# Optimization experiments

Measured on AMD Instinct MI355X. Metric: run time of the kernel, lower is better.

The kernel has to match this reference:

```python
import jax, jax.numpy as jnp
import numpy as np

FRAME_LEN = 512
HOP_LEN = 128
FFT_SIZE = 512
N_SAMPLES = -1  # TF slice [:, :-1] drops the final sample
B, FRAMES, BINS = 16, 4000, FFT_SIZE // 2 + 1


def _inverse_window():
    # tf.signal.hann_window (periodic): 0.5 - 0.5*cos(2*pi*n/N)
    n = jnp.arange(FRAME_LEN, dtype=jnp.float32)
    win = 0.5 - 0.5 * jnp.cos(2.0 * np.pi * n / FRAME_LEN)
    # tf.signal.inverse_stft_window_fn: divide by overlap-added squared window
    denom = win * win
    overlaps = -(-FRAME_LEN // HOP_LEN)  # ceil div
    denom = jnp.pad(denom, (0, overlaps * HOP_LEN - FRAME_LEN))
    denom = denom.reshape(overlaps, HOP_LEN).sum(axis=0)  # [HOP_LEN]
    denom = jnp.tile(denom, overlaps)[:FRAME_LEN]
    return win / denom


def setup_inputs() -> dict:
    key = jax.random.key(0)
    k1, k2 = jax.random.split(key)
    return {
        "stft_real": jax.random.normal(k1, (B, FRAMES, BINS), dtype=jnp.float32),
        "stft_imag": jax.random.normal(k2, (B, FRAMES, BINS), dtype=jnp.float32),
    }


def reference(stft_real, stft_imag):
    stfts = jax.lax.complex(stft_real, stft_imag)  # [B, F, BINS] complex64
    # per-frame inverse real FFT, truncate to frame_length
    frames = jnp.fft.irfft(stfts, n=FFT_SIZE, axis=-1)[..., :FRAME_LEN]  # [B, F, L] float32
    frames = frames * _inverse_window()  # broadcast window over [B, F, L]
    out_len = (FRAMES - 1) * HOP_LEN + FRAME_LEN
    # overlap-add via vectorized scatter-accumulate
    idx = jnp.arange(FRAMES)[:, None] * HOP_LEN + jnp.arange(FRAME_LEN)[None, :]  # [F, L]
    sig = jnp.zeros((B, out_len), dtype=jnp.float32).at[:, idx].add(frames)
    return sig[:, :N_SAMPLES]
```

## Files before the change

kernel.cpp:

```cpp
#include <hip/hip_runtime.h>
#include <math.h>

#define HOP       128
#define NFFT      512
#define NBINS     257
#define NFRAMES   4000
#define NB        16
#define OUT_LEN   512383
#define CPR       16
#define RPB       251
#define NCHUNK    4003
#define SP        66
#define SQ        65
#define PBUF      528

__device__ __forceinline__ void dft8_inv(const float* xr, const float* xi,
                                         float* yr, float* yi)
{
    const float C = 0.70710678118654752f;
    float ar[8], ai[8];
    ar[0]=xr[0]+xr[4]; ai[0]=xi[0]+xi[4];
    ar[1]=xr[1]+xr[5]; ai[1]=xi[1]+xi[5];
    ar[2]=xr[2]+xr[6]; ai[2]=xi[2]+xi[6];
    ar[3]=xr[3]+xr[7]; ai[3]=xi[3]+xi[7];
    float t0r=xr[0]-xr[4], t0i=xi[0]-xi[4];
    float t1r=xr[1]-xr[5], t1i=xi[1]-xi[5];
    float t2r=xr[2]-xr[6], t2i=xi[2]-xi[6];
    float t3r=xr[3]-xr[7], t3i=xi[3]-xi[7];
    ar[4]= t0r;            ai[4]= t0i;
    ar[5]= C*(t1r-t1i);    ai[5]= C*(t1r+t1i);
    ar[6]=-t2i;            ai[6]= t2r;
    ar[7]=-C*(t3r+t3i);    ai[7]= C*(t3r-t3i);
    float br[8], bi[8];
    br[0]=ar[0]+ar[2]; bi[0]=ai[0]+ai[2];
    br[1]=ar[1]+ar[3]; bi[1]=ai[1]+ai[3];
    br[2]=ar[0]-ar[2]; bi[2]=ai[0]-ai[2];
    { float u=ar[1]-ar[3], v=ai[1]-ai[3]; br[3]=-v; bi[3]=u; }
    br[4]=ar[4]+ar[6]; bi[4]=ai[4]+ai[6];
    br[5]=ar[5]+ar[7]; bi[5]=ai[5]+ai[7];
    br[6]=ar[4]-ar[6]; bi[6]=ai[4]-ai[6];
    { float u=ar[5]-ar[7], v=ai[5]-ai[7]; br[7]=-v; bi[7]=u; }
    yr[0]=br[0]+br[1]; yi[0]=bi[0]+bi[1];
    yr[4]=br[0]-br[1]; yi[4]=bi[0]-bi[1];
    yr[2]=br[2]+br[3]; yi[2]=bi[2]+bi[3];
    yr[6]=br[2]-br[3]; yi[6]=bi[2]-bi[3];
    yr[1]=br[4]+br[5]; yi[1]=bi[4]+bi[5];
    yr[5]=br[4]-br[5]; yi[5]=bi[4]-bi[5];
    yr[3]=br[6]+br[7]; yi[3]=bi[6]+bi[7];
    yr[7]=br[6]-br[7]; yi[7]=bi[6]-bi[7];
}

__global__ __launch_bounds__(256)
void istft_r8_kernel(const float* __restrict__ re,
                     const float* __restrict__ im,
                     float* __restrict__ out)
{
    __shared__ float  wtab[NFFT];
    __shared__ float2 pbuf[4][PBUF];

    const int tid = threadIdx.x;
    const int wv  = tid >> 6;
    const int l   = tid & 63;

    for (int n = tid; n < NFFT; n += 256) {
        const float wn = 0.5f - 0.5f * __cosf(6.2831853071795864f * (float)n * (1.0f/512.0f));
        const int p = n & (HOP - 1);
        float denom = 0.0f;
        #pragma unroll
        for (int o = 0; o < 4; ++o) {
            const float w2 = 0.5f - 0.5f * __cosf(6.2831853071795864f * (float)(o*HOP + p) * (1.0f/512.0f));
            denom += w2 * w2;
        }
        wtab[n] = wn / (512.0f * denom);
    }
    __syncthreads();

    float2* P = pbuf[wv];

    const int rid = blockIdx.x * 4 + wv;
    const int b   = rid / RPB;
    const int rr  = rid - b * RPB;
    const int c0  = rr * CPR;
    const int fend = min(c0 + CPR - 1, NCHUNK - 1);

    const float* __restrict__ reb = re + (size_t)b * NFRAMES * NBINS;
    const float* __restrict__ imb = im + (size_t)b * NFRAMES * NBINS;
    float* __restrict__ outb = out + (size_t)b * OUT_LEN;

    float s1r[8], s1i[8];
    {
        float sr, cr;
        __sincosf(6.2831853071795864f * (float)l * (1.0f/512.0f), &sr, &cr);
        s1r[0] = 1.0f; s1i[0] = 0.0f; s1r[1] = cr; s1i[1] = sr;
        #pragma unroll
        for (int k = 2; k < 8; ++k) {
            s1r[k] = s1r[k-1]*cr - s1i[k-1]*sr;
            s1i[k] = s1r[k-1]*sr + s1i[k-1]*cr;
        }
    }
    float s2r[8], s2i[8];
    {
        float sr, cr;
        __sincosf(6.2831853071795864f * (float)(l & 7) * (1.0f/64.0f), &sr, &cr);
        s2r[0] = 1.0f; s2i[0] = 0.0f; s2r[1] = cr; s2i[1] = sr;
        #pragma unroll
        for (int k = 2; k < 8; ++k) {
            s2r[k] = s2r[k-1]*cr - s2i[k-1]*sr;
            s2i[k] = s2r[k-1]*sr + s2i[k-1]*cr;
        }
    }
    float ww[8];
    #pragma unroll
    for (int m1 = 0; m1 < 8; ++m1) ww[m1] = wtab[l + 64*m1];

    float acc[8];
    #pragma unroll
    for (int r = 0; r < 8; ++r) acc[r] = 0.0f;

    const int n0s = l >> 3, gs = l & 7;
    const int m0t = l >> 3, n0t = l & 7;

    for (int f = c0 - 3; f <= fend; ++f) {
        if (f >= 0 && f < NFRAMES) {
            const float* __restrict__ rb = reb + (size_t)f * NBINS;
            const float* __restrict__ ib = imb + (size_t)f * NBINS;

            float xr[8], xi[8];
            #pragma unroll
            for (int a = 0; a < 8; ++a) {
                const int t  = 64*a + l;
                const int tt = (t <= 256) ? t : (512 - t);
                const float sg = (t <= 256) ? 1.0f : -1.0f;
                xr[a] = rb[tt];
                xi[a] = sg * ib[tt];
            }

            float pr[8], pi[8];
            dft8_inv(xr, xi, pr, pi);
            #pragma unroll
            for (int n0 = 0; n0 < 8; ++n0) {
                const float tr = pr[n0]*s1r[n0] - pi[n0]*s1i[n0];
                const float ti = pr[n0]*s1i[n0] + pi[n0]*s1r[n0];
                P[SP*n0 + l] = make_float2(tr, ti);
            }
            __builtin_amdgcn_wave_barrier();

            #pragma unroll
            for (int e = 0; e < 8; ++e) {
                const float2 v = P[SP*n0s + 8*e + gs];
                xr[e] = v.x; xi[e] = v.y;
            }
            __builtin_amdgcn_wave_barrier();
            float qr[8], qi[8];
            dft8_inv(xr, xi, qr, qi);
            #pragma unroll
            for (int m0 = 0; m0 < 8; ++m0) {
                const float tr = qr[m0]*s2r[m0] - qi[m0]*s2i[m0];
                const float ti = qr[m0]*s2i[m0] + qi[m0]*s2r[m0];
                P[SQ*m0 + l] = make_float2(tr, ti);
            }
            __builtin_amdgcn_wave_barrier();

            #pragma unroll
            for (int g = 0; g < 8; ++g) {
                const float2 v = P[SQ*m0t + 8*n0t + g];
                xr[g] = v.x; xi[g] = v.y;
            }
            __builtin_amdgcn_wave_barrier();
            float yr[8], yi[8];
            dft8_inv(xr, xi, yr, yi);

            #pragma unroll
            for (int m1 = 0; m1 < 8; ++m1) acc[m1] += yr[m1] * ww[m1];
        }

        if (f >= c0) {
            const int pos0 = f * HOP + l;
            const int pos1 = pos0 + 64;
            outb[pos0] = acc[0];
            if (pos1 < OUT_LEN) outb[pos1] = acc[1];
        }

        #pragma unroll
        for (int r = 0; r < 6; ++r) acc[r] = acc[r + 2];
        acc[6] = 0.0f; acc[7] = 0.0f;
    }
}

extern "C" void kernel_launch(void* const* d_in, const int* in_sizes, int n_in,
                              void* d_out, int out_size, void* d_ws, size_t ws_size,
                              hipStream_t stream) {
    (void)in_sizes; (void)n_in; (void)d_ws; (void)ws_size; (void)out_size;
    const float* re = (const float*)d_in[0];
    const float* im = (const float*)d_in[1];
    float* out = (float*)d_out;

    const int nblocks = (NB * RPB) / 4;
    istft_r8_kernel<<<dim3(nblocks), dim3(256), 0, stream>>>(re, im, out);
}
```

Baseline: 177.4 us.

## Halve chunks per wave, compute window in registers, repad LDS transposes

Frames per wave-row drop from 16 to 8, which doubles the number of waves. Each wave still recomputes 3 halo frames, so the redundant fraction of FFT work grows, but the launch now fills the GPU better. The shared window table and its block-wide barrier are replaced by a per-thread closed-form window built with a rotation recurrence. This uses the constant 1/768, since the overlap-added squared Hann window sums to 1.5. The second LDS transpose gets a padded layout (stride 9 within rows of 72) to cut bank conflicts, and the first four bin loads skip the mirror-index select.

```diff
diff --git a/kernel.cpp b/kernel.cpp
--- a/kernel.cpp
+++ b/kernel.cpp
@@ -7,12 +7,13 @@
 #define NFRAMES   4000
 #define NB        16
 #define OUT_LEN   512383
-#define CPR       16
-#define RPB       251
+#define CPR       8
+#define RPB       501
 #define NCHUNK    4003
-#define SP        66
-#define SQ        65
-#define PBUF      528
+#define SP        72
+#define SQB       72
+#define SQN       9
+#define PBUF      576
 
 __device__ __forceinline__ void dft8_inv(const float* xr, const float* xi,
                                          float* yr, float* yi)
@@ -55,25 +56,11 @@
                      const float* __restrict__ im,
                      float* __restrict__ out)
 {
-    __shared__ float  wtab[NFFT];
     __shared__ float2 pbuf[4][PBUF];
 
     const int tid = threadIdx.x;
     const int wv  = tid >> 6;
     const int l   = tid & 63;
-
-    for (int n = tid; n < NFFT; n += 256) {
-        const float wn = 0.5f - 0.5f * __cosf(6.2831853071795864f * (float)n * (1.0f/512.0f));
-        const int p = n & (HOP - 1);
-        float denom = 0.0f;
-        #pragma unroll
-        for (int o = 0; o < 4; ++o) {
-            const float w2 = 0.5f - 0.5f * __cosf(6.2831853071795864f * (float)(o*HOP + p) * (1.0f/512.0f));
-            denom += w2 * w2;
-        }
-        wtab[n] = wn / (512.0f * denom);
-    }
-    __syncthreads();
 
     float2* P = pbuf[wv];
 
@@ -109,9 +96,21 @@
             s2i[k] = s2r[k-1]*sr + s2i[k-1]*cr;
         }
     }
+
     float ww[8];
-    #pragma unroll
-    for (int m1 = 0; m1 < 8; ++m1) ww[m1] = wtab[l + 64*m1];
+    {
+        float sn, cs;
+        __sincosf(6.2831853071795864f * (float)l * (1.0f/512.0f), &sn, &cs);
+        const float R = 0.70710678118654752f;
+        float c = cs, s = sn;
+        #pragma unroll
+        for (int m1 = 0; m1 < 8; ++m1) {
+            ww[m1] = (0.5f - 0.5f * c) * (1.0f/768.0f);
+            const float cn = (c - s) * R;
+            const float sn2 = (s + c) * R;
+            c = cn; s = sn2;
+        }
+    }
 
     float acc[8];
     #pragma unroll
@@ -127,7 +126,12 @@
 
             float xr[8], xi[8];
             #pragma unroll
-            for (int a = 0; a < 8; ++a) {
+            for (int a = 0; a < 4; ++a) {
+                xr[a] = rb[64*a + l];
+                xi[a] = ib[64*a + l];
+            }
+            #pragma unroll
+            for (int a = 4; a < 8; ++a) {
                 const int t  = 64*a + l;
                 const int tt = (t <= 256) ? t : (512 - t);
                 const float sg = (t <= 256) ? 1.0f : -1.0f;
@@ -157,13 +161,13 @@
             for (int m0 = 0; m0 < 8; ++m0) {
                 const float tr = qr[m0]*s2r[m0] - qi[m0]*s2i[m0];
                 const float ti = qr[m0]*s2i[m0] + qi[m0]*s2r[m0];
-                P[SQ*m0 + l] = make_float2(tr, ti);
+                P[SQB*m0 + SQN*n0s + gs] = make_float2(tr, ti);
             }
             __builtin_amdgcn_wave_barrier();
 
             #pragma unroll
             for (int g = 0; g < 8; ++g) {
-                const float2 v = P[SQ*m0t + 8*n0t + g];
+                const float2 v = P[SQB*m0t + SQN*n0t + g];
                 xr[g] = v.x; xi[g] = v.y;
             }
             __builtin_amdgcn_wave_barrier();
```

New measurement: 179.3 us. Within noise of the previous version (+1.1%).
